# Performance work log

Hardware: AMD Instinct MI355X
Metric: run time of the kernel (lower is better)

The kernel has to match this reference:

```python
import jax, jax.numpy as jnp
import numpy as np

N0, N1, N2 = 80000, 40000, 20000
E1, E2 = 500000, 250000
FIN = 128        # in_channels
H = 2            # heads
C1 = 64          # hidden_channels -> layer1 out per head (concat -> 128)
C2 = 64          # out_channels -> layer2 out per head (mean over heads)
ED = 10          # edge_dim per embedding, total edge feat = 2*ED = 20
NTYPE, NTS = 23, 1158


def setup_inputs() -> dict:
    key = jax.random.key(0)
    ks = jax.random.split(key, 48)
    sc = 0.05
    inp = {
        "x": jax.random.normal(ks[0], (N0, FIN), jnp.float32),
        "ei1_src": jax.random.randint(ks[1], (E1,), 0, N0),
        "ei1_dst": jax.random.randint(ks[2], (E1,), 0, N1),
        "et1": jax.random.randint(ks[3], (E1,), 0, NTYPE),
        "ets1": jax.random.randint(ks[4], (E1,), 0, NTS),
        "ei2_src": jax.random.randint(ks[5], (E2,), 0, N1),
        "ei2_dst": jax.random.randint(ks[6], (E2,), 0, N2),
        "et2": jax.random.randint(ks[7], (E2,), 0, NTYPE),
        "ets2": jax.random.randint(ks[8], (E2,), 0, NTS),
        # shared edge embeddings (Linear(23,10), Linear(1158,10))
        "edge_W": jax.random.normal(ks[9], (ED, NTYPE), jnp.float32) * sc,
        "edge_b": jax.random.normal(ks[10], (ED,), jnp.float32) * sc,
        "time_W": jax.random.normal(ks[11], (ED, NTS), jnp.float32) * sc,
        "time_b": jax.random.normal(ks[12], (ED,), jnp.float32) * sc,
    }
    # layer 1: in=128, heads=2, C=64, concat=True (out dim 128)
    hc1 = H * C1
    inp["Wq1"] = jax.random.normal(ks[13], (hc1, FIN), jnp.float32) * sc
    inp["bq1"] = jnp.zeros((hc1,), jnp.float32)
    inp["Wk1"] = jax.random.normal(ks[14], (hc1, FIN), jnp.float32) * sc
    inp["bk1"] = jnp.zeros((hc1,), jnp.float32)
    inp["Wv1"] = jax.random.normal(ks[15], (hc1, FIN), jnp.float32) * sc
    inp["bv1"] = jnp.zeros((hc1,), jnp.float32)
    inp["We1"] = jax.random.normal(ks[16], (hc1, 2 * ED), jnp.float32) * sc
    inp["Wskip1"] = jax.random.normal(ks[17], (hc1, FIN), jnp.float32) * sc
    inp["bskip1"] = jnp.zeros((hc1,), jnp.float32)
    inp["Wbeta1"] = jax.random.normal(ks[18], (1, 3 * hc1), jnp.float32) * sc
    inp["ln_g"] = jnp.ones((hc1,), jnp.float32)
    inp["ln_b"] = jnp.zeros((hc1,), jnp.float32)
    # layer 2: in=128, heads=2, C=64, concat=False (out dim 64)
    hc2 = H * C2
    inp["Wq2"] = jax.random.normal(ks[19], (hc2, hc1), jnp.float32) * sc
    inp["bq2"] = jnp.zeros((hc2,), jnp.float32)
    inp["Wk2"] = jax.random.normal(ks[20], (hc2, hc1), jnp.float32) * sc
    inp["bk2"] = jnp.zeros((hc2,), jnp.float32)
    inp["Wv2"] = jax.random.normal(ks[21], (hc2, hc1), jnp.float32) * sc
    inp["bv2"] = jnp.zeros((hc2,), jnp.float32)
    inp["We2"] = jax.random.normal(ks[22], (hc2, 2 * ED), jnp.float32) * sc
    inp["Wskip2"] = jax.random.normal(ks[23], (C2, hc1), jnp.float32) * sc
    inp["bskip2"] = jnp.zeros((C2,), jnp.float32)
    inp["Wbeta2"] = jax.random.normal(ks[24], (1, 3 * C2), jnp.float32) * sc
    return inp


def _edge_feat(et, ets, edge_W, edge_b, time_W, time_b):
    # one_hot(e) @ W.T + b == W.T[e] + b (avoids materializing huge one-hot)
    return jnp.concatenate([jnp.take(edge_W.T, et, axis=0) + edge_b,
                            jnp.take(time_W.T, ets, axis=0) + time_b], axis=-1)


def _conv(x_src, x_dst, src, dst, ef, Wq, bq, Wk, bk, Wv, bv, We,
          Wskip, bskip, Wbeta, concat):
    n_dst = x_dst.shape[0]
    HC = Wq.shape[0]
    C = HC // H
    q = (x_dst @ Wq.T + bq).reshape(n_dst, H, C)            # [Nd,H,C]
    k = (x_src @ Wk.T + bk)[src].reshape(-1, H, C)          # [E,H,C]
    v = (x_src @ Wv.T + bv)[src].reshape(-1, H, C)
    e = (ef @ We.T).reshape(-1, H, C)
    k = k + e
    alpha = jnp.einsum('ehc,ehc->eh', q[dst], k) / np.sqrt(C).astype(np.float32)
    # segment softmax over destination nodes
    m = jax.ops.segment_max(alpha, dst, num_segments=n_dst)
    ex = jnp.exp(alpha - m[dst])
    s = jax.ops.segment_sum(ex, dst, num_segments=n_dst)
    a = ex / (s[dst] + 1e-16)                               # [E,H]
    msg = (v + e) * a[..., None]                            # [E,H,C]
    out = jax.ops.segment_sum(msg.reshape(-1, HC), dst, num_segments=n_dst)
    out = out if concat else out.reshape(n_dst, H, C).mean(axis=1)
    x_r = x_dst @ Wskip.T + bskip
    beta = jax.nn.sigmoid(
        jnp.concatenate([out, x_r, out - x_r], axis=-1) @ Wbeta.T)  # [Nd,1]
    return beta * x_r + (1.0 - beta) * out


def _layernorm(x, g, b):
    mu = x.mean(-1, keepdims=True)
    var = x.var(-1, keepdims=True)
    return (x - mu) / jnp.sqrt(var + 1e-5) * g + b


def reference(x, ei1_src, ei1_dst, et1, ets1, ei2_src, ei2_dst, et2, ets2,
              edge_W, edge_b, time_W, time_b,
              Wq1, bq1, Wk1, bk1, Wv1, bv1, We1, Wskip1, bskip1, Wbeta1,
              ln_g, ln_b,
              Wq2, bq2, Wk2, bk2, Wv2, bv2, We2, Wskip2, bskip2, Wbeta2):
    ef1 = _edge_feat(et1, ets1, edge_W, edge_b, time_W, time_b)
    h = _conv(x, x[:N1], ei1_src, ei1_dst, ef1,
              Wq1, bq1, Wk1, bk1, Wv1, bv1, We1, Wskip1, bskip1, Wbeta1,
              concat=True)
    h = jax.nn.gelu(_layernorm(h, ln_g, ln_b), approximate=False)
    ef2 = _edge_feat(et2, ets2, edge_W, edge_b, time_W, time_b)
    o = _conv(h, h[:N2], ei2_src, ei2_dst, ef2,
              Wq2, bq2, Wk2, bk2, Wv2, bv2, We2, Wskip2, bskip2, Wbeta2,
              concat=False)
    return jax.nn.log_softmax(o, axis=-1)
```

## Files before the change

kernel.cpp:

```cpp
#include <hip/hip_runtime.h>
#include <math.h>

#define N0 80000
#define N1 40000
#define N2 20000
#define E1C 500000
#define E2C 250000
#define NTYPE 23
#define NTS 1158

#define NB1 157
#define NB2 79
#define KV1B 1250
#define QR1B 625
#define CNTB 2930
#define KV2B 625
#define QR2B 313
#define FILLB 2930

#define OFF_XB    0u
#define OFF_QR1   5120000u
#define OFF_KV1   15360000u
#define OFF_H     25600000u
#define OFF_QR2   28160000u
#define OFF_KV2   32000000u
#define OFF_WB1   37120000u
#define OFF_BP1   37160000u
#define OFF_WB2   37170000u
#define OFF_BP2   37200000u
#define OFF_TA1   37210000u
#define OFF_TB1   37213000u
#define OFF_TA2   37370000u
#define OFF_TB2   37373000u
#define OFF_RP1   37530000u
#define OFF_CUR1  37580000u
#define OFF_ED1   37630000u
#define OFF_BS1   38640000u
#define OFF_RP2   38650000u
#define OFF_CUR2  38680000u
#define OFF_ED2   38710000u
#define OFF_BS2   39220000u
#define OFF_DONE  39230000u
#define OFF_RK1   39240000u
#define OFF_RK2   39740000u

typedef __bf16 bf16x8 __attribute__((ext_vector_type(8)));
typedef float f32x4 __attribute__((ext_vector_type(4)));

static __device__ __forceinline__ float b2f(unsigned short u) {
    union { unsigned int i; float f; } c;
    c.i = ((unsigned int)u) << 16;
    return c.f;
}
static __device__ __forceinline__ unsigned short f2b(float f) {
    unsigned int u = __float_as_uint(f);
    unsigned int r = (u + 0x7fffu + ((u >> 16) & 1u)) >> 16;
    return (unsigned short)r;
}
static __device__ __forceinline__ bf16x8 ldfrag(const unsigned short* p) {
    return *reinterpret_cast<const bf16x8*>(p);
}

static __device__ __forceinline__ void stage16(const void* g, void* l) {
    __builtin_amdgcn_global_load_lds(
        (const __attribute__((address_space(1))) unsigned int*)g,
        (__attribute__((address_space(3))) unsigned int*)l,
        16, 0, 0);
}

template <int CTRL>
static __device__ __forceinline__ float dpp_addstep(float v) {
    int x = __builtin_amdgcn_mov_dpp(__float_as_int(v), CTRL, 0xF, 0xF, true);
    return v + __int_as_float(x);
}
static __device__ __forceinline__ float red16(float v) {
    v = dpp_addstep<0xB1>(v);
    v = dpp_addstep<0x4E>(v);
    v = dpp_addstep<0x141>(v);
    v = dpp_addstep<0x140>(v);
    return v;
}
template <int CTRL>
static __device__ __forceinline__ float dpp_maxstep(float v) {
    int x = __builtin_amdgcn_mov_dpp(__float_as_int(v), CTRL, 0xF, 0xF, true);
    return fmaxf(v, __int_as_float(x));
}
static __device__ __forceinline__ float red16max(float v) {
    v = dpp_maxstep<0xB1>(v);
    v = dpp_maxstep<0x4E>(v);
    v = dpp_maxstep<0x141>(v);
    v = dpp_maxstep<0x140>(v);
    return v;
}

#define LDSS 136
#define SMEM_USHORTS 16384

template <int NTILES>
static __device__ __forceinline__ void dev_gemm_bf16out(
    const unsigned short* __restrict__ XB, const unsigned short* __restrict__ WB,
    const float* __restrict__ BP, unsigned short* __restrict__ Y, int n, int blk,
    unsigned short* sb) {
    constexpr int COLS = NTILES * 16;
    constexpr int HALF = NTILES / 2;
    constexpr int HCOLS = HALF * 16;
    constexpr int NCHUNK = (NTILES + 7) / 8;
    int wave = threadIdx.x >> 6, lane = threadIdx.x & 63;
    int m = lane & 15, quad = lane >> 4;
    int rowbase = blk * 64 + wave * 16;
    int arow = rowbase + m; if (arow >= n) arow = n - 1;
    unsigned short* swave = sb + wave * 16 * LDSS;
    const unsigned short* xrow = XB + (size_t)arow * 128 + quad * 8;
    bf16x8 a0 = ldfrag(xrow), a1 = ldfrag(xrow + 32);
    bf16x8 a2 = ldfrag(xrow + 64), a3 = ldfrag(xrow + 96);
    f32x4 acc[NTILES];
#pragma unroll
    for (int t = 0; t < NTILES; t++) acc[t] = (f32x4){0.f, 0.f, 0.f, 0.f};
    const char* gstage = (const char*)WB + wave * 1024 + lane * 16;
    char* lstage = (char*)sb + wave * 1024;
#pragma unroll
    for (int c = 0; c < NCHUNK; c++) {
#pragma unroll
        for (int i = 0; i < 8; i++)
            if (c * 8 + i < NTILES)
                stage16(gstage + (size_t)(c * 8 + i) * 4096, lstage + i * 4096);
        __syncthreads();
#pragma unroll
        for (int t = 0; t < 8; t++) {
            if (c * 8 + t < NTILES) {
                constexpr int unused = 0; (void)unused;
                int tt = c * 8 + t;
                const unsigned short* wt = sb + t * 2048 + lane * 8;
                acc[tt] = __builtin_amdgcn_mfma_f32_16x16x32_bf16(a0, ldfrag(wt), acc[tt], 0, 0, 0);
                acc[tt] = __builtin_amdgcn_mfma_f32_16x16x32_bf16(a1, ldfrag(wt + 512), acc[tt], 0, 0, 0);
                acc[tt] = __builtin_amdgcn_mfma_f32_16x16x32_bf16(a2, ldfrag(wt + 1024), acc[tt], 0, 0, 0);
                acc[tt] = __builtin_amdgcn_mfma_f32_16x16x32_bf16(a3, ldfrag(wt + 1536), acc[tt], 0, 0, 0);
            }
        }
        __syncthreads();
    }
    int tswz_bit = (quad >> 1) & 1;
#pragma unroll
    for (int half = 0; half < 2; half++) {
#pragma unroll
        for (int t = 0; t < HALF; t++) {
            int tt = half * HALF + t;
            int tsw = t ^ tswz_bit;
            float b = BP[tt * 16 + m];
#pragma unroll
            for (int r = 0; r < 4; r++)
                swave[(quad * 4 + r) * LDSS + tsw * 16 + m] = f2b(acc[tt][r] + b);
        }
#pragma unroll
        for (int i = 0; i < 4; i++) {
            int idx = i * 64 + lane;
            int r = idx / (HCOLS / 8), g = idx % (HCOLS / 8);
            int gs = g ^ (((r >> 3) & 1) << 1);
            int grow = rowbase + r;
            if (grow < n) {
                uint4 v = *(const uint4*)&swave[r * LDSS + gs * 8];
                *(uint4*)(Y + (size_t)grow * COLS + half * HCOLS + g * 8) = v;
            }
        }
    }
}

template <int NTILES>
static __device__ __forceinline__ void dev_gemm_f32out(
    const unsigned short* __restrict__ XB, const unsigned short* __restrict__ WB,
    const float* __restrict__ BP, float* __restrict__ Y, int n, int blk,
    unsigned short* sb) {
    constexpr int COLS = NTILES * 16;
    constexpr int NCHUNK = (NTILES + 7) / 8;
    int wave = threadIdx.x >> 6, lane = threadIdx.x & 63;
    int m = lane & 15, quad = lane >> 4;
    int rowbase = blk * 64 + wave * 16;
    int arow = rowbase + m; if (arow >= n) arow = n - 1;
    const unsigned short* xrow = XB + (size_t)arow * 128 + quad * 8;
    bf16x8 a0 = ldfrag(xrow), a1 = ldfrag(xrow + 32);
    bf16x8 a2 = ldfrag(xrow + 64), a3 = ldfrag(xrow + 96);
    f32x4 acc[NTILES];
#pragma unroll
    for (int t = 0; t < NTILES; t++) acc[t] = (f32x4){0.f, 0.f, 0.f, 0.f};
    const char* gstage = (const char*)WB + wave * 1024 + lane * 16;
    char* lstage = (char*)sb + wave * 1024;
#pragma unroll
    for (int c = 0; c < NCHUNK; c++) {
#pragma unroll
        for (int i = 0; i < 8; i++)
            if (c * 8 + i < NTILES)
                stage16(gstage + (size_t)(c * 8 + i) * 4096, lstage + i * 4096);
        __syncthreads();
#pragma unroll
        for (int t = 0; t < 8; t++) {
            if (c * 8 + t < NTILES) {
                int tt = c * 8 + t;
                const unsigned short* wt = sb + t * 2048 + lane * 8;
                acc[tt] = __builtin_amdgcn_mfma_f32_16x16x32_bf16(a0, ldfrag(wt), acc[tt], 0, 0, 0);
                acc[tt] = __builtin_amdgcn_mfma_f32_16x16x32_bf16(a1, ldfrag(wt + 512), acc[tt], 0, 0, 0);
                acc[tt] = __builtin_amdgcn_mfma_f32_16x16x32_bf16(a2, ldfrag(wt + 1024), acc[tt], 0, 0, 0);
                acc[tt] = __builtin_amdgcn_mfma_f32_16x16x32_bf16(a3, ldfrag(wt + 1536), acc[tt], 0, 0, 0);
            }
        }
        __syncthreads();
    }
#pragma unroll
    for (int t = 0; t < NTILES; t++) {
        float b = BP[t * 16 + m];
#pragma unroll
        for (int r = 0; r < 4; r++) {
            int grow = rowbase + quad * 4 + r;
            if (grow < n) Y[(size_t)grow * COLS + t * 16 + m] = acc[t][r] + b;
        }
    }
}

__global__ __launch_bounds__(256) void prep(
    const float* __restrict__ x, unsigned short* __restrict__ XB,
    const float* __restrict__ Wk1, const float* __restrict__ Wv1,
    const float* __restrict__ Wq1, const float* __restrict__ Wskip1,
    const float* __restrict__ bk1, const float* __restrict__ bv1,
    const float* __restrict__ bq1, const float* __restrict__ bskip1,
    const float* __restrict__ Wk2, const float* __restrict__ Wv2,
    const float* __restrict__ Wq2, const float* __restrict__ Wskip2,
    const float* __restrict__ bk2, const float* __restrict__ bv2,
    const float* __restrict__ bq2, const float* __restrict__ bskip2,
    unsigned short* __restrict__ WB1, float* __restrict__ BP1,
    unsigned short* __restrict__ WB2, float* __restrict__ BP2,
    const float* __restrict__ edge_W, const float* __restrict__ edge_b,
    const float* __restrict__ time_W, const float* __restrict__ time_b,
    const float* __restrict__ We1, const float* __restrict__ We2,
    float* __restrict__ TA1, float* __restrict__ TB1,
    float* __restrict__ TA2, float* __restrict__ TB2,
    int* __restrict__ cnt1, int* __restrict__ cnt2, int* __restrict__ done) {
    int tid = blockIdx.x * blockDim.x + threadIdx.x;
    int stride = gridDim.x * blockDim.x;
    for (int i = tid; i < N0 * 32; i += stride) {
        float4 v = *(const float4*)(x + (size_t)i * 4);
        ushort4 u;
        u.x = f2b(v.x); u.y = f2b(v.y); u.z = f2b(v.z); u.w = f2b(v.w);
        *(ushort4*)(XB + (size_t)i * 4) = u;
    }
    for (int i = tid; i < 512 * 128; i += stride) {
        int j = i & 7, l = (i >> 3) & 63, ks = (i >> 9) & 3, t = i >> 11;
        int row = t * 16 + (l & 15);
        int col = ks * 32 + ((l >> 4) & 3) * 8 + j;
        const float* w; int off;
        if (row < 128) { w = Wk1; off = 0; }
        else if (row < 256) { w = Wv1; off = 128; }
        else if (row < 384) { w = Wq1; off = 256; }
        else { w = Wskip1; off = 384; }
        WB1[i] = f2b(w[(size_t)(row - off) * 128 + col]);
    }
    for (int i = tid; i < 512; i += stride) {
        const float* b; int off;
        if (i < 128) { b = bk1; off = 0; }
        else if (i < 256) { b = bv1; off = 128; }
        else if (i < 384) { b = bq1; off = 256; }
        else { b = bskip1; off = 384; }
        BP1[i] = b[i - off];
    }
    for (int i = tid; i < 448 * 128; i += stride) {
        int j = i & 7, l = (i >> 3) & 63, ks = (i >> 9) & 3, t = i >> 11;
        int row = t * 16 + (l & 15);
        int col = ks * 32 + ((l >> 4) & 3) * 8 + j;
        const float* w; int off;
        if (row < 128) { w = Wk2; off = 0; }
        else if (row < 256) { w = Wv2; off = 128; }
        else if (row < 384) { w = Wq2; off = 256; }
        else { w = Wskip2; off = 384; }
        WB2[i] = f2b(w[(size_t)(row - off) * 128 + col]);
    }
    for (int i = tid; i < 448; i += stride) {
        const float* b; int off;
        if (i < 128) { b = bk2; off = 0; }
        else if (i < 256) { b = bv2; off = 128; }
        else if (i < 384) { b = bq2; off = 256; }
        else { b = bskip2; off = 384; }
        BP2[i] = b[i - off];
    }
    const int TBL = (NTYPE + NTS) * 128;
    for (int i = tid; i < TBL; i += stride) {
        if (i < NTYPE * 128) {
            int e = i >> 7, c = i & 127;
            float s1 = 0.f, s2 = 0.f;
#pragma unroll
            for (int j = 0; j < 10; j++) {
                float fj = edge_W[j * NTYPE + e] + edge_b[j];
                s1 += fj * We1[c * 20 + j];
                s2 += fj * We2[c * 20 + j];
            }
            TA1[i] = s1; TA2[i] = s2;
        } else {
            int u = i - NTYPE * 128;
            int ts = u >> 7, c = u & 127;
            float s1 = 0.f, s2 = 0.f;
#pragma unroll
            for (int j = 0; j < 10; j++) {
                float fj = time_W[j * NTS + ts] + time_b[j];
                s1 += fj * We1[c * 20 + 10 + j];
                s2 += fj * We2[c * 20 + 10 + j];
            }
            TB1[u] = s1; TB2[u] = s2;
        }
    }
    for (int i = tid; i < N1 + N2 + 2; i += stride) {
        if (i < N1) cnt1[i] = 0;
        else if (i < N1 + N2) cnt2[i - N1] = 0;
        else done[i - N1 - N2] = 0;
    }
}

__global__ __launch_bounds__(256) void mega_l1(
    const unsigned short* __restrict__ XB,
    const unsigned short* __restrict__ WB1, const float* __restrict__ BP1,
    unsigned short* __restrict__ KV1, float* __restrict__ QR1,
    const int* __restrict__ d1, const int* __restrict__ d2,
    int* __restrict__ cnt1, int* __restrict__ cnt2,
    int* __restrict__ rk1, int* __restrict__ rk2) {
    __shared__ __align__(16) unsigned short sbuf[SMEM_USHORTS];
    int b = blockIdx.x;
    if (b < CNTB) {
        int t = b * 256 + threadIdx.x;
        if (t < E1C) rk1[t] = atomicAdd(&cnt1[d1[t]], 1);
        else {
            t -= E1C;
            if (t < E2C) rk2[t] = atomicAdd(&cnt2[d2[t]], 1);
        }
    } else if (b < CNTB + KV1B) {
        dev_gemm_bf16out<16>(XB, WB1, BP1, KV1, N0, b - CNTB, sbuf);
    } else {
        dev_gemm_f32out<16>(XB, WB1 + 256 * 128, BP1 + 256, QR1, N1,
                            b - CNTB - KV1B, sbuf);
    }
}

__global__ __launch_bounds__(256) void gemm_l2(
    const unsigned short* __restrict__ H,
    const unsigned short* __restrict__ WB2, const float* __restrict__ BP2,
    unsigned short* __restrict__ KV2, float* __restrict__ QR2) {
    __shared__ __align__(16) unsigned short sbuf[SMEM_USHORTS];
    int b = blockIdx.x;
    if (b < KV2B) dev_gemm_bf16out<16>(H, WB2, BP2, KV2, N1, b, sbuf);
    else dev_gemm_f32out<12>(H, WB2 + 256 * 128, BP2 + 256, QR2, N2, b - KV2B, sbuf);
}

__global__ __launch_bounds__(256) void csr_scan(
    int* __restrict__ cnt1, int* __restrict__ bs1, int* __restrict__ rp1,
    int* __restrict__ cnt2, int* __restrict__ bs2, int* __restrict__ rp2,
    int* __restrict__ done) {
    __shared__ int s[256];
    __shared__ int amlast;
    int b = blockIdx.x;
    int* cnt; int* bs; int* rp; int n, lb;
    if (b < NB1) { cnt = cnt1; bs = bs1; rp = rp1; n = N1; lb = b; }
    else { cnt = cnt2; bs = bs2; rp = rp2; n = N2; lb = b - NB1; }
    int t = lb * 256 + threadIdx.x;
    int v = (t < n) ? cnt[t] : 0;
    s[threadIdx.x] = v;
    __syncthreads();
    for (int off = 128; off; off >>= 1) {
        if (threadIdx.x < off) s[threadIdx.x] += s[threadIdx.x + off];
        __syncthreads();
    }
    if (threadIdx.x == 0) {
        atomicExch(&bs[lb], s[0]);
        __threadfence();
        int prev = atomicAdd(&done[0], 1);
        amlast = (prev == NB1 + NB2 - 1) ? 1 : 0;
    }
    __syncthreads();
    if (amlast) {
        int tt = threadIdx.x;
        int v1 = (tt < NB1) ? atomicAdd(&bs1[tt], 0) : 0;
        s[tt] = v1;
        __syncthreads();
        for (int off = 1; off < 256; off <<= 1) {
            int u = (tt >= off) ? s[tt - off] : 0;
            __syncthreads();
            s[tt] += u;
            __syncthreads();
        }
        if (tt < NB1) atomicExch(&bs1[tt], s[tt] - v1);
        __syncthreads();
        int v2 = (tt < NB2) ? atomicAdd(&bs2[tt], 0) : 0;
        s[tt] = v2;
        __syncthreads();
        for (int off = 1; off < 256; off <<= 1) {
            int u = (tt >= off) ? s[tt - off] : 0;
            __syncthreads();
            s[tt] += u;
            __syncthreads();
        }
        if (tt < NB2) atomicExch(&bs2[tt], s[tt] - v2);
        __threadfence();
        __syncthreads();
        if (tt == 0) atomicExch(&done[1], 1);
    }
    if (threadIdx.x == 0) {
        while (atomicAdd(&done[1], 0) == 0) __builtin_amdgcn_s_sleep(1);
    }
    __syncthreads();
    __threadfence();
    int base = atomicAdd(&bs[lb], 0);
    s[threadIdx.x] = v;
    __syncthreads();
    for (int off = 1; off < 256; off <<= 1) {
        int u = (threadIdx.x >= off) ? s[threadIdx.x - off] : 0;
        __syncthreads();
        s[threadIdx.x] += u;
        __syncthreads();
    }
    int incl = s[threadIdx.x];
    if (t < n) rp[t] = base + incl - v;
    if (t == n - 1) rp[n] = base + incl;
}

__global__ __launch_bounds__(256) void fill_both(
    const int* __restrict__ d1, const int* __restrict__ s1,
    const int* __restrict__ et1, const int* __restrict__ ets1,
    const int* __restrict__ rp1, const int* __restrict__ rk1, uint2* __restrict__ ed1,
    const int* __restrict__ d2, const int* __restrict__ s2,
    const int* __restrict__ et2, const int* __restrict__ ets2,
    const int* __restrict__ rp2, const int* __restrict__ rk2, uint2* __restrict__ ed2) {
    int t = blockIdx.x * 256 + threadIdx.x;
    if (t < E1C) {
        int pos = rp1[d1[t]] + rk1[t];
        ed1[pos] = make_uint2((unsigned)s1[t],
                              (unsigned)(et1[t] | (ets1[t] << 16)));
    } else {
        t -= E1C;
        if (t < E2C) {
            int pos = rp2[d2[t]] + rk2[t];
            ed2[pos] = make_uint2((unsigned)s2[t],
                                  (unsigned)(et2[t] | (ets2[t] << 16)));
        }
    }
}

__global__ __launch_bounds__(256) void agg_layer1(
    const int* __restrict__ rowptr, const uint2* __restrict__ ED,
    const float* __restrict__ TA, const float* __restrict__ TB,
    const float* __restrict__ QR, const unsigned short* __restrict__ KV,
    const float* __restrict__ Wbeta,
    const float* __restrict__ ln_g, const float* __restrict__ ln_b,
    unsigned short* __restrict__ hout, int n) {
    int wid = (blockIdx.x * blockDim.x + threadIdx.x) >> 6;
    int lane = threadIdx.x & 63;
    if (wid >= n) return;
    int s = lane >> 5, cg = lane & 15;
    int co = ((lane >> 4) & 1) * 64 + 4 * cg;
    int beg = rowptr[wid], end = rowptr[wid + 1];
    float4 q4 = *(const float4*)(QR + (size_t)wid * 256 + co);
    float ax = 0.f, ay = 0.f, az = 0.f, aw = 0.f, suma = 0.f;
    int p = beg + s;
    if (p < end) {
        uint2 d0 = ED[p];
        int pA = p + 2;  bool mA = pA < end;
        uint2 d1 = ED[mA ? pA : beg];
        int pB = p + 4;  bool mB = pB < end;
        uint2 d2 = ED[mB ? pB : beg];
        int sn0 = (int)d0.x, t0 = (int)(d0.y & 0xFFFF), ts0 = (int)(d0.y >> 16);
        float4 ta0 = *(const float4*)(TA + t0 * 128 + co);
        float4 tb0 = *(const float4*)(TB + ts0 * 128 + co);
        const unsigned short* kv0 = KV + (size_t)sn0 * 256;
        ushort4 ku0 = *(const ushort4*)(kv0 + co);
        ushort4 vu0 = *(const ushort4*)(kv0 + 128 + co);
        int sn1 = (int)d1.x, t1 = (int)(d1.y & 0xFFFF), ts1 = (int)(d1.y >> 16);
        float4 ta1 = *(const float4*)(TA + t1 * 128 + co);
        float4 tb1 = *(const float4*)(TB + ts1 * 128 + co);
        const unsigned short* kv1 = KV + (size_t)sn1 * 256;
        ushort4 ku1 = *(const ushort4*)(kv1 + co);
        ushort4 vu1 = *(const ushort4*)(kv1 + 128 + co);
        for (;;) {
            int pC = pB + 2; bool mC = pC < end;
            uint2 d3 = ED[mC ? pC : beg];
            int sn2 = (int)d2.x, t2 = (int)(d2.y & 0xFFFF), ts2 = (int)(d2.y >> 16);
            float4 ta2 = *(const float4*)(TA + t2 * 128 + co);
            float4 tb2 = *(const float4*)(TB + ts2 * 128 + co);
            const unsigned short* kv2 = KV + (size_t)sn2 * 256;
            ushort4 ku2 = *(const ushort4*)(kv2 + co);
            ushort4 vu2 = *(const ushort4*)(kv2 + 128 + co);
            float e0c = ta0.x + tb0.x, e1c = ta0.y + tb0.y;
            float e2c = ta0.z + tb0.z, e3c = ta0.w + tb0.w;
            float pp = q4.x * (b2f(ku0.x) + e0c) + q4.y * (b2f(ku0.y) + e1c)
                     + q4.z * (b2f(ku0.z) + e2c) + q4.w * (b2f(ku0.w) + e3c);
            pp = red16(pp);
            float a = __expf(pp * 0.125f);
            ax += a * (b2f(vu0.x) + e0c); ay += a * (b2f(vu0.y) + e1c);
            az += a * (b2f(vu0.z) + e2c); aw += a * (b2f(vu0.w) + e3c);
            suma += a;
            if (!mA) break;
            ta0 = ta1; tb0 = tb1; ku0 = ku1; vu0 = vu1;
            ta1 = ta2; tb1 = tb2; ku1 = ku2; vu1 = vu2;
            d2 = d3;
            mA = mB; mB = mC; pB = pC;
        }
    }
    ax += __shfl_xor(ax, 32); ay += __shfl_xor(ay, 32);
    az += __shfl_xor(az, 32); aw += __shfl_xor(aw, 32);
    suma += __shfl_xor(suma, 32);
    float inv_s = 1.f / (suma + 1e-16f);
    float ox = ax * inv_s, oy = ay * inv_s, oz = az * inv_s, ow = aw * inv_s;
    float4 r4 = *(const float4*)(QR + (size_t)wid * 256 + 128 + co);
    float4 wo = *(const float4*)(Wbeta + co);
    float4 wr = *(const float4*)(Wbeta + 128 + co);
    float4 wd = *(const float4*)(Wbeta + 256 + co);
    float pb = wo.x * ox + wr.x * r4.x + wd.x * (ox - r4.x)
             + wo.y * oy + wr.y * r4.y + wd.y * (oy - r4.y)
             + wo.z * oz + wr.z * r4.z + wd.z * (oz - r4.z)
             + wo.w * ow + wr.w * r4.w + wd.w * (ow - r4.w);
    pb = red16(pb);
    pb += __shfl_xor(pb, 16);
    float beta = 1.f / (1.f + __expf(-pb));
    float gx = beta * r4.x + (1.f - beta) * ox;
    float gy = beta * r4.y + (1.f - beta) * oy;
    float gz = beta * r4.z + (1.f - beta) * oz;
    float gw = beta * r4.w + (1.f - beta) * ow;
    float sm = gx + gy + gz + gw;
    float sq = gx * gx + gy * gy + gz * gz + gw * gw;
    sm = red16(sm); sm += __shfl_xor(sm, 16);
    sq = red16(sq); sq += __shfl_xor(sq, 16);
    float mu = sm * (1.f / 128.f);
    float var = sq * (1.f / 128.f) - mu * mu;
    float inv = rsqrtf(var + 1e-5f);
    float4 lg = *(const float4*)(ln_g + co);
    float4 lb = *(const float4*)(ln_b + co);
    float yx = (gx - mu) * inv * lg.x + lb.x;
    float yy = (gy - mu) * inv * lg.y + lb.y;
    float yz = (gz - mu) * inv * lg.z + lb.z;
    float yw = (gw - mu) * inv * lg.w + lb.w;
    const float ISQ2 = 0.70710678118654752f;
    yx = 0.5f * yx * (1.f + erff(yx * ISQ2));
    yy = 0.5f * yy * (1.f + erff(yy * ISQ2));
    yz = 0.5f * yz * (1.f + erff(yz * ISQ2));
    yw = 0.5f * yw * (1.f + erff(yw * ISQ2));
    if (s == 0) {
        ushort4 hv;
        hv.x = f2b(yx); hv.y = f2b(yy); hv.z = f2b(yz); hv.w = f2b(yw);
        *(ushort4*)(hout + (size_t)wid * 128 + co) = hv;
    }
}

__global__ __launch_bounds__(256) void agg_layer2(
    const int* __restrict__ rowptr, const uint2* __restrict__ ED,
    const float* __restrict__ TA, const float* __restrict__ TB,
    const float* __restrict__ QR, const unsigned short* __restrict__ KV,
    const float* __restrict__ Wbeta,
    float* __restrict__ o, int n) {
    int wid = (blockIdx.x * blockDim.x + threadIdx.x) >> 6;
    int lane = threadIdx.x & 63;
    if (wid >= n) return;
    int s = lane >> 5, cg = lane & 15;
    int co = ((lane >> 4) & 1) * 64 + 4 * cg;
    int beg = rowptr[wid], end = rowptr[wid + 1];
    float4 q4 = *(const float4*)(QR + (size_t)wid * 192 + co);
    float ax = 0.f, ay = 0.f, az = 0.f, aw = 0.f, suma = 0.f;
    int p = beg + s;
    if (p < end) {
        uint2 d0 = ED[p];
        int pA = p + 2;  bool mA = pA < end;
        uint2 d1 = ED[mA ? pA : beg];
        int pB = p + 4;  bool mB = pB < end;
        uint2 d2 = ED[mB ? pB : beg];
        int sn0 = (int)d0.x, t0 = (int)(d0.y & 0xFFFF), ts0 = (int)(d0.y >> 16);
        float4 ta0 = *(const float4*)(TA + t0 * 128 + co);
        float4 tb0 = *(const float4*)(TB + ts0 * 128 + co);
        const unsigned short* kv0 = KV + (size_t)sn0 * 256;
        ushort4 ku0 = *(const ushort4*)(kv0 + co);
        ushort4 vu0 = *(const ushort4*)(kv0 + 128 + co);
        int sn1 = (int)d1.x, t1 = (int)(d1.y & 0xFFFF), ts1 = (int)(d1.y >> 16);
        float4 ta1 = *(const float4*)(TA + t1 * 128 + co);
        float4 tb1 = *(const float4*)(TB + ts1 * 128 + co);
        const unsigned short* kv1 = KV + (size_t)sn1 * 256;
        ushort4 ku1 = *(const ushort4*)(kv1 + co);
        ushort4 vu1 = *(const ushort4*)(kv1 + 128 + co);
        for (;;) {
            int pC = pB + 2; bool mC = pC < end;
            uint2 d3 = ED[mC ? pC : beg];
            int sn2 = (int)d2.x, t2 = (int)(d2.y & 0xFFFF), ts2 = (int)(d2.y >> 16);
            float4 ta2 = *(const float4*)(TA + t2 * 128 + co);
            float4 tb2 = *(const float4*)(TB + ts2 * 128 + co);
            const unsigned short* kv2 = KV + (size_t)sn2 * 256;
            ushort4 ku2 = *(const ushort4*)(kv2 + co);
            ushort4 vu2 = *(const ushort4*)(kv2 + 128 + co);
            float e0c = ta0.x + tb0.x, e1c = ta0.y + tb0.y;
            float e2c = ta0.z + tb0.z, e3c = ta0.w + tb0.w;
            float pp = q4.x * (b2f(ku0.x) + e0c) + q4.y * (b2f(ku0.y) + e1c)
                     + q4.z * (b2f(ku0.z) + e2c) + q4.w * (b2f(ku0.w) + e3c);
            pp = red16(pp);
            float a = __expf(pp * 0.125f);
            ax += a * (b2f(vu0.x) + e0c); ay += a * (b2f(vu0.y) + e1c);
            az += a * (b2f(vu0.z) + e2c); aw += a * (b2f(vu0.w) + e3c);
            suma += a;
            if (!mA) break;
            ta0 = ta1; tb0 = tb1; ku0 = ku1; vu0 = vu1;
            ta1 = ta2; tb1 = tb2; ku1 = ku2; vu1 = vu2;
            d2 = d3;
            mA = mB; mB = mC; pB = pC;
        }
    }
    ax += __shfl_xor(ax, 32); ay += __shfl_xor(ay, 32);
    az += __shfl_xor(az, 32); aw += __shfl_xor(aw, 32);
    suma += __shfl_xor(suma, 32);
    float inv_s = 1.f / (suma + 1e-16f);
    float ox = ax * inv_s, oy = ay * inv_s, oz = az * inv_s, ow = aw * inv_s;
    ox = 0.5f * (ox + __shfl_xor(ox, 16));
    oy = 0.5f * (oy + __shfl_xor(oy, 16));
    oz = 0.5f * (oz + __shfl_xor(oz, 16));
    ow = 0.5f * (ow + __shfl_xor(ow, 16));
    float4 r4 = *(const float4*)(QR + (size_t)wid * 192 + 128 + 4 * cg);
    float4 wo = *(const float4*)(Wbeta + 4 * cg);
    float4 wr = *(const float4*)(Wbeta + 64 + 4 * cg);
    float4 wd = *(const float4*)(Wbeta + 128 + 4 * cg);
    float pb = wo.x * ox + wr.x * r4.x + wd.x * (ox - r4.x)
             + wo.y * oy + wr.y * r4.y + wd.y * (oy - r4.y)
             + wo.z * oz + wr.z * r4.z + wd.z * (oz - r4.z)
             + wo.w * ow + wr.w * r4.w + wd.w * (ow - r4.w);
    pb = red16(pb);
    float beta = 1.f / (1.f + __expf(-pb));
    float vx = beta * r4.x + (1.f - beta) * ox;
    float vy = beta * r4.y + (1.f - beta) * oy;
    float vz = beta * r4.z + (1.f - beta) * oz;
    float vw = beta * r4.w + (1.f - beta) * ow;
    float m = fmaxf(fmaxf(vx, vy), fmaxf(vz, vw));
    m = red16max(m);
    float se = __expf(vx - m) + __expf(vy - m) + __expf(vz - m) + __expf(vw - m);
    se = red16(se);
    float lse = m + logf(se);
    if (lane < 16)
        *(float4*)(o + (size_t)wid * 64 + 4 * cg) =
            make_float4(vx - lse, vy - lse, vz - lse, vw - lse);
}

extern "C" void kernel_launch(void* const* d_in, const int* in_sizes, int n_in,
                              void* d_out, int out_size, void* d_ws, size_t ws_size,
                              hipStream_t stream) {
    const float* x        = (const float*)d_in[0];
    const int*   ei1_src  = (const int*)d_in[1];
    const int*   ei1_dst  = (const int*)d_in[2];
    const int*   et1      = (const int*)d_in[3];
    const int*   ets1     = (const int*)d_in[4];
    const int*   ei2_src  = (const int*)d_in[5];
    const int*   ei2_dst  = (const int*)d_in[6];
    const int*   et2      = (const int*)d_in[7];
    const int*   ets2     = (const int*)d_in[8];
    const float* edge_W   = (const float*)d_in[9];
    const float* edge_b   = (const float*)d_in[10];
    const float* time_W   = (const float*)d_in[11];
    const float* time_b   = (const float*)d_in[12];
    const float* Wq1      = (const float*)d_in[13];
    const float* bq1      = (const float*)d_in[14];
    const float* Wk1      = (const float*)d_in[15];
    const float* bk1      = (const float*)d_in[16];
    const float* Wv1      = (const float*)d_in[17];
    const float* bv1      = (const float*)d_in[18];
    const float* We1      = (const float*)d_in[19];
    const float* Wskip1   = (const float*)d_in[20];
    const float* bskip1   = (const float*)d_in[21];
    const float* Wbeta1   = (const float*)d_in[22];
    const float* ln_g     = (const float*)d_in[23];
    const float* ln_b     = (const float*)d_in[24];
    const float* Wq2      = (const float*)d_in[25];
    const float* bq2      = (const float*)d_in[26];
    const float* Wk2      = (const float*)d_in[27];
    const float* bk2      = (const float*)d_in[28];
    const float* Wv2      = (const float*)d_in[29];
    const float* bv2      = (const float*)d_in[30];
    const float* We2      = (const float*)d_in[31];
    const float* Wskip2   = (const float*)d_in[32];
    const float* bskip2   = (const float*)d_in[33];
    const float* Wbeta2   = (const float*)d_in[34];

    float* ws = (float*)d_ws;
    unsigned short* xb  = (unsigned short*)(ws + OFF_XB);
    float* qr1          = ws + OFF_QR1;
    unsigned short* kv1 = (unsigned short*)(ws + OFF_KV1);
    unsigned short* h   = (unsigned short*)(ws + OFF_H);
    float* qr2          = ws + OFF_QR2;
    unsigned short* kv2 = (unsigned short*)(ws + OFF_KV2);
    unsigned short* wb1 = (unsigned short*)(ws + OFF_WB1);
    float* bp1          = ws + OFF_BP1;
    unsigned short* wb2 = (unsigned short*)(ws + OFF_WB2);
    float* bp2          = ws + OFF_BP2;
    float* ta1          = ws + OFF_TA1;
    float* tb1          = ws + OFF_TB1;
    float* ta2          = ws + OFF_TA2;
    float* tb2          = ws + OFF_TB2;
    int*   rp1          = (int*)(ws + OFF_RP1);
    int*   cur1         = (int*)(ws + OFF_CUR1);
    uint2* ed1          = (uint2*)(ws + OFF_ED1);
    int*   bs1          = (int*)(ws + OFF_BS1);
    int*   rp2          = (int*)(ws + OFF_RP2);
    int*   cur2         = (int*)(ws + OFF_CUR2);
    uint2* ed2          = (uint2*)(ws + OFF_ED2);
    int*   bs2          = (int*)(ws + OFF_BS2);
    int*   done         = (int*)(ws + OFF_DONE);
    int*   rk1          = (int*)(ws + OFF_RK1);
    int*   rk2          = (int*)(ws + OFF_RK2);

    prep<<<2048, 256, 0, stream>>>(
        x, xb,
        Wk1, Wv1, Wq1, Wskip1, bk1, bv1, bq1, bskip1,
        Wk2, Wv2, Wq2, Wskip2, bk2, bv2, bq2, bskip2,
        wb1, bp1, wb2, bp2,
        edge_W, edge_b, time_W, time_b, We1, We2,
        ta1, tb1, ta2, tb2, cur1, cur2, done);
    mega_l1<<<KV1B + QR1B + CNTB, 256, 0, stream>>>(
        xb, wb1, bp1, kv1, qr1, ei1_dst, ei2_dst, cur1, cur2, rk1, rk2);
    csr_scan<<<NB1 + NB2, 256, 0, stream>>>(cur1, bs1, rp1, cur2, bs2, rp2, done);
    fill_both<<<FILLB, 256, 0, stream>>>(
        ei1_dst, ei1_src, et1, ets1, rp1, rk1, ed1,
        ei2_dst, ei2_src, et2, ets2, rp2, rk2, ed2);
    agg_layer1<<<(N1 + 3) / 4, 256, 0, stream>>>(rp1, ed1,
        ta1, tb1, qr1, kv1, Wbeta1, ln_g, ln_b, h, N1);
    gemm_l2<<<KV2B + QR2B, 256, 0, stream>>>(h, wb2, bp2, kv2, qr2);
    agg_layer2<<<(N2 + 3) / 4, 256, 0, stream>>>(rp2, ed2,
        ta2, tb2, qr2, kv2, Wbeta2, (float*)d_out, N2);
}
```

Baseline: 350.3 us.

## Remap aggregation lanes to 8 channels each with four parallel edge groups

Both attention aggregation kernels now give each lane 8 contiguous channels, loaded with 16-byte gathers, instead of 4 channels. Each 16-lane group covers all 128 channels of one edge, so a wave processes four edges per step rather than two. The per-edge dot-product reduction drops to 8 lanes, and the four group partials are combined with two shuffles after the loop. The goal is fewer, wider gather loads and more edges in flight per wave, at the cost of more registers per lane and more idle lanes on low-degree nodes.

```diff
diff --git a/kernel.cpp b/kernel.cpp
--- a/kernel.cpp
+++ b/kernel.cpp
@@ -46,11 +46,18 @@
 
 typedef __bf16 bf16x8 __attribute__((ext_vector_type(8)));
 typedef float f32x4 __attribute__((ext_vector_type(4)));
+typedef float f32x2 __attribute__((ext_vector_type(2)));
 
 static __device__ __forceinline__ float b2f(unsigned short u) {
     union { unsigned int i; float f; } c;
     c.i = ((unsigned int)u) << 16;
     return c.f;
+}
+static __device__ __forceinline__ f32x2 b2f2(unsigned int u) {
+    f32x2 r;
+    r.x = __uint_as_float(u << 16);
+    r.y = __uint_as_float(u & 0xFFFF0000u);
+    return r;
 }
 static __device__ __forceinline__ unsigned short f2b(float f) {
     unsigned int u = __float_as_uint(f);
@@ -80,16 +87,21 @@
     v = dpp_addstep<0x140>(v);
     return v;
 }
+static __device__ __forceinline__ float red8(float v) {
+    v = dpp_addstep<0xB1>(v);
+    v = dpp_addstep<0x4E>(v);
+    v = dpp_addstep<0x141>(v);
+    return v;
+}
 template <int CTRL>
 static __device__ __forceinline__ float dpp_maxstep(float v) {
     int x = __builtin_amdgcn_mov_dpp(__float_as_int(v), CTRL, 0xF, 0xF, true);
     return fmaxf(v, __int_as_float(x));
 }
-static __device__ __forceinline__ float red16max(float v) {
+static __device__ __forceinline__ float red8max(float v) {
     v = dpp_maxstep<0xB1>(v);
     v = dpp_maxstep<0x4E>(v);
     v = dpp_maxstep<0x141>(v);
-    v = dpp_maxstep<0x140>(v);
     return v;
 }
 
@@ -128,7 +140,6 @@
 #pragma unroll
         for (int t = 0; t < 8; t++) {
             if (c * 8 + t < NTILES) {
-                constexpr int unused = 0; (void)unused;
                 int tt = c * 8 + t;
                 const unsigned short* wt = sb + t * 2048 + lane * 8;
                 acc[tt] = __builtin_amdgcn_mfma_f32_16x16x32_bf16(a0, ldfrag(wt), acc[tt], 0, 0, 0);
@@ -438,6 +449,69 @@
     }
 }
 
+static __device__ __forceinline__ void edge_accum(
+    int beg, int end, int eg, int co, float4 qA, float4 qB,
+    const uint2* __restrict__ ED, const float* __restrict__ TA,
+    const float* __restrict__ TB, const unsigned short* __restrict__ KV,
+    float4& accA, float4& accB, float& suma) {
+    int p = beg + eg;
+    if (p >= end) return;
+
+    uint2 d0 = ED[p];
+    int pA = p + 4;  bool mA = pA < end;
+    uint2 d1 = ED[mA ? pA : beg];
+    int pB = p + 8;  bool mB = pB < end;
+    uint2 d2 = ED[mB ? pB : beg];
+
+    float4 eA0, eB0, eA1, eB1, eA2, eB2;
+    uint4 ku0, vu0, ku1, vu1, ku2, vu2;
+
+#define LOADSET4(S, D) { \
+    int t_ = (int)(D.y & 0xFFFF), ts_ = (int)(D.y >> 16); \
+    const float* ta_ = TA + t_ * 128 + co; \
+    const float* tb_ = TB + ts_ * 128 + co; \
+    float4 a0_ = *(const float4*)ta_, a1_ = *(const float4*)(ta_ + 4); \
+    float4 b0_ = *(const float4*)tb_, b1_ = *(const float4*)(tb_ + 4); \
+    eA##S = make_float4(a0_.x + b0_.x, a0_.y + b0_.y, a0_.z + b0_.z, a0_.w + b0_.w); \
+    eB##S = make_float4(a1_.x + b1_.x, a1_.y + b1_.y, a1_.z + b1_.z, a1_.w + b1_.w); \
+    const unsigned short* kv_ = KV + (size_t)D.x * 256 + co; \
+    ku##S = *(const uint4*)kv_; \
+    vu##S = *(const uint4*)(kv_ + 128); }
+
+    LOADSET4(0, d0)
+    LOADSET4(1, d1)
+    for (;;) {
+        int pC = pB + 4; bool mC = pC < end;
+        uint2 d3 = ED[mC ? pC : beg];
+        LOADSET4(2, d2)
+        {
+            f32x2 k01 = b2f2(ku0.x), k23 = b2f2(ku0.y);
+            f32x2 k45 = b2f2(ku0.z), k67 = b2f2(ku0.w);
+            float pp = qA.x * (k01.x + eA0.x) + qA.y * (k01.y + eA0.y)
+                     + qA.z * (k23.x + eA0.z) + qA.w * (k23.y + eA0.w)
+                     + qB.x * (k45.x + eB0.x) + qB.y * (k45.y + eB0.y)
+                     + qB.z * (k67.x + eB0.z) + qB.w * (k67.y + eB0.w);
+            pp = red8(pp);
+            float a = __expf(pp * 0.125f);
+            f32x2 v01 = b2f2(vu0.x), v23 = b2f2(vu0.y);
+            f32x2 v45 = b2f2(vu0.z), v67 = b2f2(vu0.w);
+            accA.x += a * (v01.x + eA0.x); accA.y += a * (v01.y + eA0.y);
+            accA.z += a * (v23.x + eA0.z); accA.w += a * (v23.y + eA0.w);
+            accB.x += a * (v45.x + eB0.x); accB.y += a * (v45.y + eB0.y);
+            accB.z += a * (v67.x + eB0.z); accB.w += a * (v67.y + eB0.w);
+            suma += a;
+        }
+        if (!mA) break;
+        eA0 = eA1; eB0 = eB1; ku0 = ku1; vu0 = vu1;
+        eA1 = eA2; eB1 = eB2; ku1 = ku2; vu1 = vu2;
+        d2 = d3;
+        mA = mB; mB = mC; pB = pC;
+    }
+#undef LOADSET4
+}
+
+#define CMB2(x) { x += __shfl_xor(x, 16); x += __shfl_xor(x, 32); }
+
 __global__ __launch_bounds__(256) void agg_layer1(
     const int* __restrict__ rowptr, const uint2* __restrict__ ED,
     const float* __restrict__ TA, const float* __restrict__ TB,
@@ -448,97 +522,84 @@
     int wid = (blockIdx.x * blockDim.x + threadIdx.x) >> 6;
     int lane = threadIdx.x & 63;
     if (wid >= n) return;
-    int s = lane >> 5, cg = lane & 15;
-    int co = ((lane >> 4) & 1) * 64 + 4 * cg;
+    int eg = lane >> 4, cg = lane & 15;
+    int co = cg * 8;
     int beg = rowptr[wid], end = rowptr[wid + 1];
-    float4 q4 = *(const float4*)(QR + (size_t)wid * 256 + co);
-    float ax = 0.f, ay = 0.f, az = 0.f, aw = 0.f, suma = 0.f;
-    int p = beg + s;
-    if (p < end) {
-        uint2 d0 = ED[p];
-        int pA = p + 2;  bool mA = pA < end;
-        uint2 d1 = ED[mA ? pA : beg];
-        int pB = p + 4;  bool mB = pB < end;
-        uint2 d2 = ED[mB ? pB : beg];
-        int sn0 = (int)d0.x, t0 = (int)(d0.y & 0xFFFF), ts0 = (int)(d0.y >> 16);
-        float4 ta0 = *(const float4*)(TA + t0 * 128 + co);
-        float4 tb0 = *(const float4*)(TB + ts0 * 128 + co);
-        const unsigned short* kv0 = KV + (size_t)sn0 * 256;
-        ushort4 ku0 = *(const ushort4*)(kv0 + co);
-        ushort4 vu0 = *(const ushort4*)(kv0 + 128 + co);
-        int sn1 = (int)d1.x, t1 = (int)(d1.y & 0xFFFF), ts1 = (int)(d1.y >> 16);
-        float4 ta1 = *(const float4*)(TA + t1 * 128 + co);
-        float4 tb1 = *(const float4*)(TB + ts1 * 128 + co);
-        const unsigned short* kv1 = KV + (size_t)sn1 * 256;
-        ushort4 ku1 = *(const ushort4*)(kv1 + co);
-        ushort4 vu1 = *(const ushort4*)(kv1 + 128 + co);
-        for (;;) {
-            int pC = pB + 2; bool mC = pC < end;
-            uint2 d3 = ED[mC ? pC : beg];
-            int sn2 = (int)d2.x, t2 = (int)(d2.y & 0xFFFF), ts2 = (int)(d2.y >> 16);
-            float4 ta2 = *(const float4*)(TA + t2 * 128 + co);
-            float4 tb2 = *(const float4*)(TB + ts2 * 128 + co);
-            const unsigned short* kv2 = KV + (size_t)sn2 * 256;
-            ushort4 ku2 = *(const ushort4*)(kv2 + co);
-            ushort4 vu2 = *(const ushort4*)(kv2 + 128 + co);
-            float e0c = ta0.x + tb0.x, e1c = ta0.y + tb0.y;
-            float e2c = ta0.z + tb0.z, e3c = ta0.w + tb0.w;
-            float pp = q4.x * (b2f(ku0.x) + e0c) + q4.y * (b2f(ku0.y) + e1c)
-                     + q4.z * (b2f(ku0.z) + e2c) + q4.w * (b2f(ku0.w) + e3c);
-            pp = red16(pp);
-            float a = __expf(pp * 0.125f);
-            ax += a * (b2f(vu0.x) + e0c); ay += a * (b2f(vu0.y) + e1c);
-            az += a * (b2f(vu0.z) + e2c); aw += a * (b2f(vu0.w) + e3c);
-            suma += a;
-            if (!mA) break;
-            ta0 = ta1; tb0 = tb1; ku0 = ku1; vu0 = vu1;
-            ta1 = ta2; tb1 = tb2; ku1 = ku2; vu1 = vu2;
-            d2 = d3;
-            mA = mB; mB = mC; pB = pC;
-        }
-    }
-    ax += __shfl_xor(ax, 32); ay += __shfl_xor(ay, 32);
-    az += __shfl_xor(az, 32); aw += __shfl_xor(aw, 32);
-    suma += __shfl_xor(suma, 32);
+    const float* qp = QR + (size_t)wid * 256 + co;
+    float4 qA = *(const float4*)qp, qB = *(const float4*)(qp + 4);
+    float4 accA = make_float4(0.f, 0.f, 0.f, 0.f);
+    float4 accB = make_float4(0.f, 0.f, 0.f, 0.f);
+    float suma = 0.f;
+    edge_accum(beg, end, eg, co, qA, qB, ED, TA, TB, KV, accA, accB, suma);
+    CMB2(accA.x) CMB2(accA.y) CMB2(accA.z) CMB2(accA.w)
+    CMB2(accB.x) CMB2(accB.y) CMB2(accB.z) CMB2(accB.w)
+    CMB2(suma)
     float inv_s = 1.f / (suma + 1e-16f);
-    float ox = ax * inv_s, oy = ay * inv_s, oz = az * inv_s, ow = aw * inv_s;
-    float4 r4 = *(const float4*)(QR + (size_t)wid * 256 + 128 + co);
-    float4 wo = *(const float4*)(Wbeta + co);
-    float4 wr = *(const float4*)(Wbeta + 128 + co);
-    float4 wd = *(const float4*)(Wbeta + 256 + co);
-    float pb = wo.x * ox + wr.x * r4.x + wd.x * (ox - r4.x)
-             + wo.y * oy + wr.y * r4.y + wd.y * (oy - r4.y)
-             + wo.z * oz + wr.z * r4.z + wd.z * (oz - r4.z)
-             + wo.w * ow + wr.w * r4.w + wd.w * (ow - r4.w);
+    float o0 = accA.x * inv_s, o1 = accA.y * inv_s;
+    float o2 = accA.z * inv_s, o3 = accA.w * inv_s;
+    float o4 = accB.x * inv_s, o5 = accB.y * inv_s;
+    float o6 = accB.z * inv_s, o7 = accB.w * inv_s;
+    const float* rp_ = QR + (size_t)wid * 256 + 128 + co;
+    float4 rA = *(const float4*)rp_, rB = *(const float4*)(rp_ + 4);
+    float4 woA = *(const float4*)(Wbeta + co);
+    float4 woB = *(const float4*)(Wbeta + co + 4);
+    float4 wrA = *(const float4*)(Wbeta + 128 + co);
+    float4 wrB = *(const float4*)(Wbeta + 128 + co + 4);
+    float4 wdA = *(const float4*)(Wbeta + 256 + co);
+    float4 wdB = *(const float4*)(Wbeta + 256 + co + 4);
+    float pb = woA.x * o0 + wrA.x * rA.x + wdA.x * (o0 - rA.x)
+             + woA.y * o1 + wrA.y * rA.y + wdA.y * (o1 - rA.y)
+             + woA.z * o2 + wrA.z * rA.z + wdA.z * (o2 - rA.z)
+             + woA.w * o3 + wrA.w * rA.w + wdA.w * (o3 - rA.w)
+             + woB.x * o4 + wrB.x * rB.x + wdB.x * (o4 - rB.x)
+             + woB.y * o5 + wrB.y * rB.y + wdB.y * (o5 - rB.y)
+             + woB.z * o6 + wrB.z * rB.z + wdB.z * (o6 - rB.z)
+             + woB.w * o7 + wrB.w * rB.w + wdB.w * (o7 - rB.w);
     pb = red16(pb);
-    pb += __shfl_xor(pb, 16);
     float beta = 1.f / (1.f + __expf(-pb));
-    float gx = beta * r4.x + (1.f - beta) * ox;
-    float gy = beta * r4.y + (1.f - beta) * oy;
-    float gz = beta * r4.z + (1.f - beta) * oz;
-    float gw = beta * r4.w + (1.f - beta) * ow;
-    float sm = gx + gy + gz + gw;
-    float sq = gx * gx + gy * gy + gz * gz + gw * gw;
-    sm = red16(sm); sm += __shfl_xor(sm, 16);
-    sq = red16(sq); sq += __shfl_xor(sq, 16);
+    float g0 = beta * rA.x + (1.f - beta) * o0;
+    float g1 = beta * rA.y + (1.f - beta) * o1;
+    float g2 = beta * rA.z + (1.f - beta) * o2;
+    float g3 = beta * rA.w + (1.f - beta) * o3;
+    float g4 = beta * rB.x + (1.f - beta) * o4;
+    float g5 = beta * rB.y + (1.f - beta) * o5;
+    float g6 = beta * rB.z + (1.f - beta) * o6;
+    float g7 = beta * rB.w + (1.f - beta) * o7;
+    float sm = g0 + g1 + g2 + g3 + g4 + g5 + g6 + g7;
+    float sq = g0 * g0 + g1 * g1 + g2 * g2 + g3 * g3
+             + g4 * g4 + g5 * g5 + g6 * g6 + g7 * g7;
+    sm = red16(sm);
+    sq = red16(sq);
     float mu = sm * (1.f / 128.f);
     float var = sq * (1.f / 128.f) - mu * mu;
     float inv = rsqrtf(var + 1e-5f);
-    float4 lg = *(const float4*)(ln_g + co);
-    float4 lb = *(const float4*)(ln_b + co);
-    float yx = (gx - mu) * inv * lg.x + lb.x;
-    float yy = (gy - mu) * inv * lg.y + lb.y;
-    float yz = (gz - mu) * inv * lg.z + lb.z;
-    float yw = (gw - mu) * inv * lg.w + lb.w;
+    float4 lgA = *(const float4*)(ln_g + co);
+    float4 lgB = *(const float4*)(ln_g + co + 4);
+    float4 lbA = *(const float4*)(ln_b + co);
+    float4 lbB = *(const float4*)(ln_b + co + 4);
+    float y0 = (g0 - mu) * inv * lgA.x + lbA.x;
+    float y1 = (g1 - mu) * inv * lgA.y + lbA.y;
+    float y2 = (g2 - mu) * inv * lgA.z + lbA.z;
+    float y3 = (g3 - mu) * inv * lgA.w + lbA.w;
+    float y4 = (g4 - mu) * inv * lgB.x + lbB.x;
+    float y5 = (g5 - mu) * inv * lgB.y + lbB.y;
+    float y6 = (g6 - mu) * inv * lgB.z + lbB.z;
+    float y7 = (g7 - mu) * inv * lgB.w + lbB.w;
     const float ISQ2 = 0.70710678118654752f;
-    yx = 0.5f * yx * (1.f + erff(yx * ISQ2));
-    yy = 0.5f * yy * (1.f + erff(yy * ISQ2));
-    yz = 0.5f * yz * (1.f + erff(yz * ISQ2));
-    yw = 0.5f * yw * (1.f + erff(yw * ISQ2));
-    if (s == 0) {
-        ushort4 hv;
-        hv.x = f2b(yx); hv.y = f2b(yy); hv.z = f2b(yz); hv.w = f2b(yw);
-        *(ushort4*)(hout + (size_t)wid * 128 + co) = hv;
+    y0 = 0.5f * y0 * (1.f + erff(y0 * ISQ2));
+    y1 = 0.5f * y1 * (1.f + erff(y1 * ISQ2));
+    y2 = 0.5f * y2 * (1.f + erff(y2 * ISQ2));
+    y3 = 0.5f * y3 * (1.f + erff(y3 * ISQ2));
+    y4 = 0.5f * y4 * (1.f + erff(y4 * ISQ2));
+    y5 = 0.5f * y5 * (1.f + erff(y5 * ISQ2));
+    y6 = 0.5f * y6 * (1.f + erff(y6 * ISQ2));
+    y7 = 0.5f * y7 * (1.f + erff(y7 * ISQ2));
+    if (eg == 0) {
+        unsigned u0 = (unsigned)f2b(y0) | ((unsigned)f2b(y1) << 16);
+        unsigned u1 = (unsigned)f2b(y2) | ((unsigned)f2b(y3) << 16);
+        unsigned u2 = (unsigned)f2b(y4) | ((unsigned)f2b(y5) << 16);
+        unsigned u3 = (unsigned)f2b(y6) | ((unsigned)f2b(y7) << 16);
+        *(uint4*)(hout + (size_t)wid * 128 + co) = make_uint4(u0, u1, u2, u3);
     }
 }
 
@@ -551,86 +612,70 @@
     int wid = (blockIdx.x * blockDim.x + threadIdx.x) >> 6;
     int lane = threadIdx.x & 63;
     if (wid >= n) return;
-    int s = lane >> 5, cg = lane & 15;
-    int co = ((lane >> 4) & 1) * 64 + 4 * cg;
+    int eg = lane >> 4, cg = lane & 15;
+    int co = cg * 8;
     int beg = rowptr[wid], end = rowptr[wid + 1];
-    float4 q4 = *(const float4*)(QR + (size_t)wid * 192 + co);
-    float ax = 0.f, ay = 0.f, az = 0.f, aw = 0.f, suma = 0.f;
-    int p = beg + s;
-    if (p < end) {
-        uint2 d0 = ED[p];
-        int pA = p + 2;  bool mA = pA < end;
-        uint2 d1 = ED[mA ? pA : beg];
-        int pB = p + 4;  bool mB = pB < end;
-        uint2 d2 = ED[mB ? pB : beg];
-        int sn0 = (int)d0.x, t0 = (int)(d0.y & 0xFFFF), ts0 = (int)(d0.y >> 16);
-        float4 ta0 = *(const float4*)(TA + t0 * 128 + co);
-        float4 tb0 = *(const float4*)(TB + ts0 * 128 + co);
-        const unsigned short* kv0 = KV + (size_t)sn0 * 256;
-        ushort4 ku0 = *(const ushort4*)(kv0 + co);
-        ushort4 vu0 = *(const ushort4*)(kv0 + 128 + co);
-        int sn1 = (int)d1.x, t1 = (int)(d1.y & 0xFFFF), ts1 = (int)(d1.y >> 16);
-        float4 ta1 = *(const float4*)(TA + t1 * 128 + co);
-        float4 tb1 = *(const float4*)(TB + ts1 * 128 + co);
-        const unsigned short* kv1 = KV + (size_t)sn1 * 256;
-        ushort4 ku1 = *(const ushort4*)(kv1 + co);
-        ushort4 vu1 = *(const ushort4*)(kv1 + 128 + co);
-        for (;;) {
-            int pC = pB + 2; bool mC = pC < end;
-            uint2 d3 = ED[mC ? pC : beg];
-            int sn2 = (int)d2.x, t2 = (int)(d2.y & 0xFFFF), ts2 = (int)(d2.y >> 16);
-            float4 ta2 = *(const float4*)(TA + t2 * 128 + co);
-            float4 tb2 = *(const float4*)(TB + ts2 * 128 + co);
-            const unsigned short* kv2 = KV + (size_t)sn2 * 256;
-            ushort4 ku2 = *(const ushort4*)(kv2 + co);
-            ushort4 vu2 = *(const ushort4*)(kv2 + 128 + co);
-            float e0c = ta0.x + tb0.x, e1c = ta0.y + tb0.y;
-            float e2c = ta0.z + tb0.z, e3c = ta0.w + tb0.w;
-            float pp = q4.x * (b2f(ku0.x) + e0c) + q4.y * (b2f(ku0.y) + e1c)
-                     + q4.z * (b2f(ku0.z) + e2c) + q4.w * (b2f(ku0.w) + e3c);
-            pp = red16(pp);
-            float a = __expf(pp * 0.125f);
-            ax += a * (b2f(vu0.x) + e0c); ay += a * (b2f(vu0.y) + e1c);
-            az += a * (b2f(vu0.z) + e2c); aw += a * (b2f(vu0.w) + e3c);
-            suma += a;
-            if (!mA) break;
-            ta0 = ta1; tb0 = tb1; ku0 = ku1; vu0 = vu1;
-            ta1 = ta2; tb1 = tb2; ku1 = ku2; vu1 = vu2;
-            d2 = d3;
-            mA = mB; mB = mC; pB = pC;
-        }
-    }
-    ax += __shfl_xor(ax, 32); ay += __shfl_xor(ay, 32);
-    az += __shfl_xor(az, 32); aw += __shfl_xor(aw, 32);
-    suma += __shfl_xor(suma, 32);
+    const float* qp = QR + (size_t)wid * 192 + co;
+    float4 qA = *(const float4*)qp, qB = *(const float4*)(qp + 4);
+    float4 accA = make_float4(0.f, 0.f, 0.f, 0.f);
+    float4 accB = make_float4(0.f, 0.f, 0.f, 0.f);
+    float suma = 0.f;
+    edge_accum(beg, end, eg, co, qA, qB, ED, TA, TB, KV, accA, accB, suma);
+    CMB2(accA.x) CMB2(accA.y) CMB2(accA.z) CMB2(accA.w)
+    CMB2(accB.x) CMB2(accB.y) CMB2(accB.z) CMB2(accB.w)
+    CMB2(suma)
     float inv_s = 1.f / (suma + 1e-16f);
-    float ox = ax * inv_s, oy = ay * inv_s, oz = az * inv_s, ow = aw * inv_s;
-    ox = 0.5f * (ox + __shfl_xor(ox, 16));
-    oy = 0.5f * (oy + __shfl_xor(oy, 16));
-    oz = 0.5f * (oz + __shfl_xor(oz, 16));
-    ow = 0.5f * (ow + __shfl_xor(ow, 16));
-    float4 r4 = *(const float4*)(QR + (size_t)wid * 192 + 128 + 4 * cg);
-    float4 wo = *(const float4*)(Wbeta + 4 * cg);
-    float4 wr = *(const float4*)(Wbeta + 64 + 4 * cg);
-    float4 wd = *(const float4*)(Wbeta + 128 + 4 * cg);
-    float pb = wo.x * ox + wr.x * r4.x + wd.x * (ox - r4.x)
-             + wo.y * oy + wr.y * r4.y + wd.y * (oy - r4.y)
-             + wo.z * oz + wr.z * r4.z + wd.z * (oz - r4.z)
-             + wo.w * ow + wr.w * r4.w + wd.w * (ow - r4.w);
-    pb = red16(pb);
+    float o0 = accA.x * inv_s, o1 = accA.y * inv_s;
+    float o2 = accA.z * inv_s, o3 = accA.w * inv_s;
+    float o4 = accB.x * inv_s, o5 = accB.y * inv_s;
+    float o6 = accB.z * inv_s, o7 = accB.w * inv_s;
+    o0 = 0.5f * (o0 + __shfl_xor(o0, 8));
+    o1 = 0.5f * (o1 + __shfl_xor(o1, 8));
+    o2 = 0.5f * (o2 + __shfl_xor(o2, 8));
+    o3 = 0.5f * (o3 + __shfl_xor(o3, 8));
+    o4 = 0.5f * (o4 + __shfl_xor(o4, 8));
+    o5 = 0.5f * (o5 + __shfl_xor(o5, 8));
+    o6 = 0.5f * (o6 + __shfl_xor(o6, 8));
+    o7 = 0.5f * (o7 + __shfl_xor(o7, 8));
+    int oc = (cg & 7) * 8;
+    const float* rp_ = QR + (size_t)wid * 192 + 128 + oc;
+    float4 rA = *(const float4*)rp_, rB = *(const float4*)(rp_ + 4);
+    float4 woA = *(const float4*)(Wbeta + oc);
+    float4 woB = *(const float4*)(Wbeta + oc + 4);
+    float4 wrA = *(const float4*)(Wbeta + 64 + oc);
+    float4 wrB = *(const float4*)(Wbeta + 64 + oc + 4);
+    float4 wdA = *(const float4*)(Wbeta + 128 + oc);
+    float4 wdB = *(const float4*)(Wbeta + 128 + oc + 4);
+    float pb = woA.x * o0 + wrA.x * rA.x + wdA.x * (o0 - rA.x)
+             + woA.y * o1 + wrA.y * rA.y + wdA.y * (o1 - rA.y)
+             + woA.z * o2 + wrA.z * rA.z + wdA.z * (o2 - rA.z)
+             + woA.w * o3 + wrA.w * rA.w + wdA.w * (o3 - rA.w)
+             + woB.x * o4 + wrB.x * rB.x + wdB.x * (o4 - rB.x)
+             + woB.y * o5 + wrB.y * rB.y + wdB.y * (o5 - rB.y)
+             + woB.z * o6 + wrB.z * rB.z + wdB.z * (o6 - rB.z)
+             + woB.w * o7 + wrB.w * rB.w + wdB.w * (o7 - rB.w);
+    pb = red8(pb);
     float beta = 1.f / (1.f + __expf(-pb));
-    float vx = beta * r4.x + (1.f - beta) * ox;
-    float vy = beta * r4.y + (1.f - beta) * oy;
-    float vz = beta * r4.z + (1.f - beta) * oz;
-    float vw = beta * r4.w + (1.f - beta) * ow;
-    float m = fmaxf(fmaxf(vx, vy), fmaxf(vz, vw));
-    m = red16max(m);
-    float se = __expf(vx - m) + __expf(vy - m) + __expf(vz - m) + __expf(vw - m);
-    se = red16(se);
-    float lse = m + logf(se);
-    if (lane < 16)
-        *(float4*)(o + (size_t)wid * 64 + 4 * cg) =
-            make_float4(vx - lse, vy - lse, vz - lse, vw - lse);
+    float v0 = beta * rA.x + (1.f - beta) * o0;
+    float v1 = beta * rA.y + (1.f - beta) * o1;
+    float v2 = beta * rA.z + (1.f - beta) * o2;
+    float v3 = beta * rA.w + (1.f - beta) * o3;
+    float v4 = beta * rB.x + (1.f - beta) * o4;
+    float v5 = beta * rB.y + (1.f - beta) * o5;
+    float v6 = beta * rB.z + (1.f - beta) * o6;
+    float v7 = beta * rB.w + (1.f - beta) * o7;
+    float mm = fmaxf(fmaxf(fmaxf(v0, v1), fmaxf(v2, v3)),
+                     fmaxf(fmaxf(v4, v5), fmaxf(v6, v7)));
+    mm = red8max(mm);
+    float se = __expf(v0 - mm) + __expf(v1 - mm) + __expf(v2 - mm) + __expf(v3 - mm)
+             + __expf(v4 - mm) + __expf(v5 - mm) + __expf(v6 - mm) + __expf(v7 - mm);
+    se = red8(se);
+    float lse = mm + logf(se);
+    if (eg == 0 && cg < 8) {
+        float* op = o + (size_t)wid * 64 + oc;
+        *(float4*)op = make_float4(v0 - lse, v1 - lse, v2 - lse, v3 - lse);
+        *(float4*)(op + 4) = make_float4(v4 - lse, v5 - lse, v6 - lse, v7 - lse);
+    }
 }
 
 extern "C" void kernel_launch(void* const* d_in, const int* in_sizes, int n_in,
```

Measured after the change: 371.9 us. 1.06x slower.
